# Optimization experiments

Hardware: AMD Instinct MI355X
Metric: run time of the kernel (lower is better)

The kernel has to match this reference:

```python
import jax, jax.numpy as jnp
import numpy as np

N_NODES = 100000
N_EDGES = 1600000
NODE_F = 8   # augmented node features
EDGE_F = 2   # augmented edge features
GLOB_F = 1
HID = 16
L = 3        # message passing steps

EDGE_IN = GLOB_F + EDGE_F + 2 * NODE_F   # 19
NODE_IN = GLOB_F + EDGE_F + NODE_F       # 11
GLOB_IN = EDGE_F + NODE_F + GLOB_F       # 11


def setup_inputs() -> dict:
    key = jax.random.key(0)
    ks = jax.random.split(key, 20)
    inp = {
        "x": jax.random.normal(ks[0], (N_NODES, NODE_F), dtype=jnp.float32),
        "edge_index": jax.random.randint(ks[1], (2, N_EDGES), 0, N_NODES, dtype=jnp.int32),
        "edge_attr": jax.random.normal(ks[2], (N_EDGES, EDGE_F), dtype=jnp.float32),
        "g": jax.random.normal(ks[3], (1, GLOB_F), dtype=jnp.float32),
    }
    s = 0.1
    inp["edge_W1"] = jax.random.normal(ks[4], (L, EDGE_IN, HID), dtype=jnp.float32) * s
    inp["edge_b1"] = jnp.zeros((L, HID), dtype=jnp.float32)
    inp["edge_W2"] = jax.random.normal(ks[5], (L, HID, EDGE_F), dtype=jnp.float32) * s
    inp["edge_b2"] = jnp.zeros((L, EDGE_F), dtype=jnp.float32)
    inp["node_W1"] = jax.random.normal(ks[6], (L, NODE_IN, HID), dtype=jnp.float32) * s
    inp["node_b1"] = jnp.zeros((L, HID), dtype=jnp.float32)
    inp["node_W2"] = jax.random.normal(ks[7], (L, HID, NODE_F), dtype=jnp.float32) * s
    inp["node_b2"] = jnp.zeros((L, NODE_F), dtype=jnp.float32)
    inp["glob_W1"] = jax.random.normal(ks[8], (L, GLOB_IN, HID), dtype=jnp.float32) * s
    inp["glob_b1"] = jnp.zeros((L, HID), dtype=jnp.float32)
    inp["glob_W2"] = jax.random.normal(ks[9], (L, HID, GLOB_F), dtype=jnp.float32) * s
    inp["glob_b2"] = jnp.zeros((L, GLOB_F), dtype=jnp.float32)
    return inp


def _mlp(h, W1, b1, W2, b2):
    # two-layer MLP with ReLU after first layer only (activate_final=False, no layer_norm)
    return jnp.maximum(h @ W1 + b1, 0.0) @ W2 + b2


def reference(x, edge_index, edge_attr, g,
              edge_W1, edge_b1, edge_W2, edge_b2,
              node_W1, node_b1, node_W2, node_b2,
              glob_W1, glob_b1, glob_W2, glob_b2):
    row, col = edge_index[0], edge_index[1]
    n = x.shape[0]
    for l in range(L):
        g_e = jnp.broadcast_to(g, (row.shape[0], GLOB_F))
        # edge block: gather node features along edges, concat, MLP -> [E, EDGE_F]
        e_in = jnp.concatenate([g_e, x[row], x[col], edge_attr], axis=1)
        edge_emb = _mlp(e_in, edge_W1[l], edge_b1[l], edge_W2[l], edge_b2[l])
        # sum-aggregate edge embeddings to source nodes
        agg = jax.ops.segment_sum(edge_emb, row, num_segments=n)
        g_n = jnp.broadcast_to(g, (n, GLOB_F))
        node_emb = _mlp(jnp.concatenate([g_n, x, agg], axis=1),
                        node_W1[l], node_b1[l], node_W2[l], node_b2[l])
        # global block on mean-aggregated edge/node embeddings
        edge_gl = jnp.mean(edge_emb, axis=0, keepdims=True)
        node_gl = jnp.mean(node_emb, axis=0, keepdims=True)
        g = _mlp(jnp.concatenate([node_gl, edge_gl, g], axis=1),
                 glob_W1[l], glob_b1[l], glob_W2[l], glob_b2[l])
        x, edge_attr = node_emb, edge_emb
    return x  # final node embeddings [N, NODE_F]
```

## Files before the change

### kernel.cpp

```cpp
#include <hip/hip_runtime.h>

#define NN 100000
#define NE 1600000
#define CH 4096
#define NCHUNK ((NE + CH - 1) / CH)
#define NBUCK ((NN + 255) / 256)

__device__ __forceinline__ float wave_red(float v) {
#pragma unroll
    for (int off = 32; off > 0; off >>= 1) v += __shfl_down(v, off, 64);
    return v;
}

__global__ __launch_bounds__(256) void hist_kernel(
    const int* __restrict__ ei, int* __restrict__ hist)
{
    __shared__ int h[NBUCK];
    int t = threadIdx.x, c = blockIdx.x;
    for (int b = t; b < NBUCK; b += 256) h[b] = 0;
    __syncthreads();
    int base = c * CH;
    for (int i = t; i < CH; i += 256) {
        int e = base + i;
        if (e < NE) atomicAdd(&h[ei[e] >> 8], 1);
    }
    __syncthreads();
    for (int b = t; b < NBUCK; b += 256) hist[c * NBUCK + b] = h[b];
}

__global__ __launch_bounds__(512) void bscan_kernel(
    const int* __restrict__ hist, int* __restrict__ baseT, int* __restrict__ colTotal)
{
    __shared__ int buf[2][512];
    int b = blockIdx.x, t = threadIdx.x;
    int v = (t < NCHUNK) ? hist[t * NBUCK + b] : 0;
    buf[0][t] = v;
    __syncthreads();
    int src = 0;
    for (int d = 1; d < 512; d <<= 1) {
        int nv = buf[src][t] + ((t >= d) ? buf[src][t - d] : 0);
        buf[src ^ 1][t] = nv;
        src ^= 1;
        __syncthreads();
    }
    if (t < NCHUNK) baseT[b * NCHUNK + t] = buf[src][t] - v;
    if (t == NCHUNK - 1) colTotal[b] = buf[src][t];
}

__global__ __launch_bounds__(512) void boff_kernel(
    const int* __restrict__ colTotal, int* __restrict__ b_off)
{
    __shared__ int buf[2][512];
    int t = threadIdx.x;
    int v = (t < NBUCK) ? colTotal[t] : 0;
    buf[0][t] = v;
    __syncthreads();
    int src = 0;
    for (int d = 1; d < 512; d <<= 1) {
        int nv = buf[src][t] + ((t >= d) ? buf[src][t - d] : 0);
        buf[src ^ 1][t] = nv;
        src ^= 1;
        __syncthreads();
    }
    if (t < NBUCK) b_off[t] = buf[src][t] - v;
    if (t == NBUCK - 1) b_off[NBUCK] = buf[src][t];
}

__global__ __launch_bounds__(256) void fillb_kernel(
    const int* __restrict__ ei, const float* __restrict__ eattr,
    const int* __restrict__ baseT, const int* __restrict__ b_off,
    float4* __restrict__ rec)
{
    __shared__ int sslot[NBUCK];
    int t = threadIdx.x, c = blockIdx.x;
    for (int b = t; b < NBUCK; b += 256)
        sslot[b] = b_off[b] + baseT[b * NCHUNK + c];
    __syncthreads();
    int base = c * CH;
    for (int i = t; i < CH; i += 256) {
        int e = base + i;
        if (e < NE) {
            int row = ei[e];
            int slot = atomicAdd(&sslot[row >> 8], 1);
            float2 ea = reinterpret_cast<const float2*>(eattr)[e];
            float4 v;
            v.x = __int_as_float(row);
            v.y = __int_as_float(ei[NE + e]);
            v.z = ea.x; v.w = ea.y;
            rec[slot] = v;
        }
    }
}

template <bool WRITE_REC, bool NEED_SUM>
__global__ __launch_bounds__(256, 4) void fused_kernel(
    float4* __restrict__ rec, const int* __restrict__ b_off,
    const float* __restrict__ gptr,
    const float* __restrict__ eW1, const float* __restrict__ eB1,
    const float* __restrict__ eW2, const float* __restrict__ eB2,
    const float* __restrict__ xin,
    const float* __restrict__ nW1, const float* __restrict__ nB1,
    const float* __restrict__ nW2, const float* __restrict__ nB2,
    float* __restrict__ xout, float* __restrict__ sums)
{
    __shared__ float sPrT[16 * 256];
    __shared__ float sagg[256][2];
    __shared__ float redE[4][2];
    __shared__ float redN[4][8];
    int tid = threadIdx.x;
    sagg[tid][0] = 0.f; sagg[tid][1] = 0.f;

    int n0 = blockIdx.x * 256;
    int nrow = n0 + tid;
    if (nrow < NN) {
        const float4* xi = reinterpret_cast<const float4*>(xin + (size_t)nrow * 8);
        float4 a0 = xi[0], a1 = xi[1];
        float xv[8] = {a0.x, a0.y, a0.z, a0.w, a1.x, a1.y, a1.z, a1.w};
        float pr[16];
#pragma unroll
        for (int q = 0; q < 16; q++) pr[q] = 0.f;
#pragma unroll
        for (int k = 0; k < 8; k++) {
            float v = xv[k];
#pragma unroll
            for (int q = 0; q < 16; q++) pr[q] += v * eW1[(1 + k) * 16 + q];
        }
#pragma unroll
        for (int q = 0; q < 16; q++) sPrT[q * 256 + tid] = pr[q];
    }
    __syncthreads();

    int e0 = b_off[blockIdx.x], e1 = b_off[blockIdx.x + 1];

    float gval = gptr[0];
    float gterm[16];
#pragma unroll
    for (int q = 0; q < 16; q++) gterm[q] = eB1[q] + gval * eW1[q];

    float t0 = 0.f, t1 = 0.f;
    for (int e = e0 + tid; e < e1; e += 256) {
        float4 r = rec[e];
        int row = __float_as_int(r.x);
        int col = __float_as_int(r.y);
        float ea0 = r.z, ea1 = r.w;
        int li = row - n0;
        const float4* xc4 = reinterpret_cast<const float4*>(xin + (size_t)col * 8);
        float4 c0 = xc4[0], c1 = xc4[1];
        float xc[8] = {c0.x, c0.y, c0.z, c0.w, c1.x, c1.y, c1.z, c1.w};
        float h[16];
#pragma unroll
        for (int q = 0; q < 16; q++) h[q] = gterm[q] + sPrT[q * 256 + li];
#pragma unroll
        for (int k = 0; k < 8; k++) {
            float v = xc[k];
#pragma unroll
            for (int q = 0; q < 16; q++) h[q] += v * eW1[(9 + k) * 16 + q];
        }
#pragma unroll
        for (int q = 0; q < 16; q++) {
            h[q] += ea0 * eW1[17 * 16 + q];
            h[q] += ea1 * eW1[18 * 16 + q];
        }
        float s0 = eB2[0], s1 = eB2[1];
#pragma unroll
        for (int q = 0; q < 16; q++) {
            float rr = fmaxf(h[q], 0.f);
            s0 += rr * eW2[2 * q];
            s1 += rr * eW2[2 * q + 1];
        }
        if (WRITE_REC) {
            float4 w;
            w.x = r.x; w.y = r.y; w.z = s0; w.w = s1;
            rec[e] = w;
        }
        atomicAdd(&sagg[li][0], s0);
        atomicAdd(&sagg[li][1], s1);
        t0 += s0; t1 += s1;
    }

    if (NEED_SUM) {
        float r0 = wave_red(t0);
        float r1 = wave_red(t1);
        int wave = tid >> 6, lane = tid & 63;
        if (lane == 0) { redE[wave][0] = r0; redE[wave][1] = r1; }
    }
    __syncthreads();
    if (NEED_SUM && tid == 0) {
        atomicAdd(&sums[0], redE[0][0] + redE[1][0] + redE[2][0] + redE[3][0]);
        atomicAdd(&sums[1], redE[0][1] + redE[1][1] + redE[2][1] + redE[3][1]);
    }

    int n = n0 + tid;
    float out[8];
#pragma unroll
    for (int m = 0; m < 8; m++) out[m] = 0.f;

    if (n < NN) {
        float in[11];
        in[0] = gval;
        const float4* xi = reinterpret_cast<const float4*>(xin + (size_t)n * 8);
        float4 a0 = xi[0], a1 = xi[1];
        in[1] = a0.x; in[2] = a0.y; in[3] = a0.z; in[4] = a0.w;
        in[5] = a1.x; in[6] = a1.y; in[7] = a1.z; in[8] = a1.w;
        in[9] = sagg[tid][0]; in[10] = sagg[tid][1];

        float h[16];
#pragma unroll
        for (int q = 0; q < 16; q++) h[q] = nB1[q];
#pragma unroll
        for (int k = 0; k < 11; k++) {
            float v = in[k];
#pragma unroll
            for (int q = 0; q < 16; q++) h[q] += v * nW1[k * 16 + q];
        }
#pragma unroll
        for (int m = 0; m < 8; m++) out[m] = nB2[m];
#pragma unroll
        for (int q = 0; q < 16; q++) {
            float hq = fmaxf(h[q], 0.f);
#pragma unroll
            for (int m = 0; m < 8; m++) out[m] += hq * nW2[q * 8 + m];
        }
        float4* xo = reinterpret_cast<float4*>(xout + (size_t)n * 8);
        xo[0] = make_float4(out[0], out[1], out[2], out[3]);
        xo[1] = make_float4(out[4], out[5], out[6], out[7]);
    }
    if (NEED_SUM) {
        float r[8];
#pragma unroll
        for (int m = 0; m < 8; m++) r[m] = wave_red(out[m]);
        int wave = tid >> 6, lane = tid & 63;
        if (lane == 0) {
#pragma unroll
            for (int m = 0; m < 8; m++) redN[wave][m] = r[m];
        }
        __syncthreads();
        if (tid == 0) {
#pragma unroll
            for (int m = 0; m < 8; m++) {
                float s = redN[0][m] + redN[1][m] + redN[2][m] + redN[3][m];
                atomicAdd(&sums[2 + m], s);
            }
        }
    }
}

__global__ void glob_kernel(const float* __restrict__ sums,
                            const float* __restrict__ gold,
                            const float* __restrict__ W1, const float* __restrict__ B1,
                            const float* __restrict__ W2, const float* __restrict__ B2,
                            float* __restrict__ gnew)
{
    if (threadIdx.x == 0 && blockIdx.x == 0) {
        float in[11];
#pragma unroll
        for (int j = 0; j < 8; j++) in[j] = sums[2 + j] * (1.0f / NN);
        in[8] = sums[0] * (1.0f / NE);
        in[9] = sums[1] * (1.0f / NE);
        in[10] = gold[0];
        float acc = B2[0];
#pragma unroll
        for (int j = 0; j < 16; j++) {
            float h = B1[j];
#pragma unroll
            for (int k = 0; k < 11; k++) h += in[k] * W1[k * 16 + j];
            acc += fmaxf(h, 0.f) * W2[j];
        }
        gnew[0] = acc;
    }
}

extern "C" void kernel_launch(void* const* d_in, const int* in_sizes, int n_in,
                              void* d_out, int out_size, void* d_ws, size_t ws_size,
                              hipStream_t stream) {
    const float* x     = (const float*)d_in[0];
    const int*   ei    = (const int*)d_in[1];
    const float* eattr = (const float*)d_in[2];
    const float* g     = (const float*)d_in[3];
    const float* eW1 = (const float*)d_in[4];
    const float* eB1 = (const float*)d_in[5];
    const float* eW2 = (const float*)d_in[6];
    const float* eB2 = (const float*)d_in[7];
    const float* nW1 = (const float*)d_in[8];
    const float* nB1 = (const float*)d_in[9];
    const float* nW2 = (const float*)d_in[10];
    const float* nB2 = (const float*)d_in[11];
    const float* gW1 = (const float*)d_in[12];
    const float* gB1 = (const float*)d_in[13];
    const float* gW2 = (const float*)d_in[14];
    const float* gB2 = (const float*)d_in[15];
    float* out = (float*)d_out;

    char* ws = (char*)d_ws;
    float*  xb0   = (float*)(ws);
    float*  xb1   = (float*)(ws + 3200000);
    int*    b_off = (int*)  (ws + 6400000);
    float*  sums  = (float*)(ws + 6401600);
    float*  g1    = (float*)(ws + 6401728);
    float*  g2    = g1 + 1;
    float4* rec   = (float4*)(ws + 6401792);
    int*    hist     = (int*)xb1;
    int*    baseT    = (int*)((char*)xb1 + 611584);
    int*    colTotal = (int*)((char*)xb1 + 1223168);

    dim3 blk(256);
    dim3 cgrid(NCHUNK);
    dim3 bgrid(NBUCK);
    dim3 ngrid((NN + 255) / 256);

    hipMemsetAsync(sums, 0, 128, stream);
    hist_kernel<<<cgrid, blk, 0, stream>>>(ei, hist);
    bscan_kernel<<<bgrid, 512, 0, stream>>>(hist, baseT, colTotal);
    boff_kernel<<<1, 512, 0, stream>>>(colTotal, b_off);
    fillb_kernel<<<cgrid, blk, 0, stream>>>(ei, eattr, baseT, b_off, rec);

    fused_kernel<true, true><<<bgrid, blk, 0, stream>>>(
        rec, b_off, g,
        eW1, eB1, eW2, eB2,
        x, nW1, nB1, nW2, nB2,
        xb0, sums);
    glob_kernel<<<1, 64, 0, stream>>>(sums, g, gW1, gB1, gW2, gB2, g1);

    fused_kernel<true, true><<<bgrid, blk, 0, stream>>>(
        rec, b_off, g1,
        eW1 + 304, eB1 + 16, eW2 + 32, eB2 + 2,
        xb0, nW1 + 176, nB1 + 16, nW2 + 128, nB2 + 8,
        xb1, sums + 16);
    glob_kernel<<<1, 64, 0, stream>>>(sums + 16, g1, gW1 + 176, gB1 + 16, gW2 + 16, gB2 + 1, g2);

    fused_kernel<false, false><<<bgrid, blk, 0, stream>>>(
        rec, b_off, g2,
        eW1 + 608, eB1 + 32, eW2 + 64, eB2 + 4,
        xb1, nW1 + 352, nB1 + 32, nW2 + 256, nB2 + 16,
        out, sums);
}
```

Measured before the change: 354.9 us.

## Replace bucket-sorted fused edge/node kernel with unsorted edge kernel plus global atomics

Drops the histogram, scan and fill passes that bucketed edges by source node. Edges are now processed in their original order by a grid-stride edge kernel that gathers both endpoint features and scatters into global agg buffers with global float atomics. A separate node kernel then reads those buffers. This removes the sort preprocessing and the per-bucket load imbalance, but adds an extra row gather per edge, global atomics, a memset of the agg buffers, and an extra launch per layer.

```diff
diff --git a/kernel.cpp b/kernel.cpp
--- a/kernel.cpp
+++ b/kernel.cpp
@@ -2,9 +2,8 @@
 
 #define NN 100000
 #define NE 1600000
-#define CH 4096
-#define NCHUNK ((NE + CH - 1) / CH)
-#define NBUCK ((NN + 255) / 256)
+#define EGRID 2048
+#define NGRID ((NN + 255) / 256)
 
 __device__ __forceinline__ float wave_red(float v) {
 #pragma unroll
@@ -12,197 +11,102 @@
     return v;
 }
 
-__global__ __launch_bounds__(256) void hist_kernel(
-    const int* __restrict__ ei, int* __restrict__ hist)
-{
-    __shared__ int h[NBUCK];
-    int t = threadIdx.x, c = blockIdx.x;
-    for (int b = t; b < NBUCK; b += 256) h[b] = 0;
-    __syncthreads();
-    int base = c * CH;
-    for (int i = t; i < CH; i += 256) {
-        int e = base + i;
-        if (e < NE) atomicAdd(&h[ei[e] >> 8], 1);
-    }
-    __syncthreads();
-    for (int b = t; b < NBUCK; b += 256) hist[c * NBUCK + b] = h[b];
-}
-
-__global__ __launch_bounds__(512) void bscan_kernel(
-    const int* __restrict__ hist, int* __restrict__ baseT, int* __restrict__ colTotal)
-{
-    __shared__ int buf[2][512];
-    int b = blockIdx.x, t = threadIdx.x;
-    int v = (t < NCHUNK) ? hist[t * NBUCK + b] : 0;
-    buf[0][t] = v;
-    __syncthreads();
-    int src = 0;
-    for (int d = 1; d < 512; d <<= 1) {
-        int nv = buf[src][t] + ((t >= d) ? buf[src][t - d] : 0);
-        buf[src ^ 1][t] = nv;
-        src ^= 1;
-        __syncthreads();
-    }
-    if (t < NCHUNK) baseT[b * NCHUNK + t] = buf[src][t] - v;
-    if (t == NCHUNK - 1) colTotal[b] = buf[src][t];
-}
-
-__global__ __launch_bounds__(512) void boff_kernel(
-    const int* __restrict__ colTotal, int* __restrict__ b_off)
-{
-    __shared__ int buf[2][512];
-    int t = threadIdx.x;
-    int v = (t < NBUCK) ? colTotal[t] : 0;
-    buf[0][t] = v;
-    __syncthreads();
-    int src = 0;
-    for (int d = 1; d < 512; d <<= 1) {
-        int nv = buf[src][t] + ((t >= d) ? buf[src][t - d] : 0);
-        buf[src ^ 1][t] = nv;
-        src ^= 1;
-        __syncthreads();
-    }
-    if (t < NBUCK) b_off[t] = buf[src][t] - v;
-    if (t == NBUCK - 1) b_off[NBUCK] = buf[src][t];
-}
-
-__global__ __launch_bounds__(256) void fillb_kernel(
-    const int* __restrict__ ei, const float* __restrict__ eattr,
-    const int* __restrict__ baseT, const int* __restrict__ b_off,
-    float4* __restrict__ rec)
-{
-    __shared__ int sslot[NBUCK];
-    int t = threadIdx.x, c = blockIdx.x;
-    for (int b = t; b < NBUCK; b += 256)
-        sslot[b] = b_off[b] + baseT[b * NCHUNK + c];
-    __syncthreads();
-    int base = c * CH;
-    for (int i = t; i < CH; i += 256) {
-        int e = base + i;
-        if (e < NE) {
-            int row = ei[e];
-            int slot = atomicAdd(&sslot[row >> 8], 1);
-            float2 ea = reinterpret_cast<const float2*>(eattr)[e];
-            float4 v;
-            v.x = __int_as_float(row);
-            v.y = __int_as_float(ei[NE + e]);
-            v.z = ea.x; v.w = ea.y;
-            rec[slot] = v;
-        }
-    }
-}
-
-template <bool WRITE_REC, bool NEED_SUM>
-__global__ __launch_bounds__(256, 4) void fused_kernel(
-    float4* __restrict__ rec, const int* __restrict__ b_off,
+template <bool WRITE_EMB, bool NEED_SUM>
+__global__ __launch_bounds__(256) void edge_kernel(
+    const int* __restrict__ ei,
+    const float2* __restrict__ eain,
+    float2* __restrict__ eout,
+    const float* __restrict__ xin,
     const float* __restrict__ gptr,
     const float* __restrict__ eW1, const float* __restrict__ eB1,
     const float* __restrict__ eW2, const float* __restrict__ eB2,
-    const float* __restrict__ xin,
+    float* __restrict__ agg, float* __restrict__ sums)
+{
+    __shared__ float redE[4][2];
+    int tid = threadIdx.x;
+    float gval = gptr[0];
+    float gterm[16];
+#pragma unroll
+    for (int q = 0; q < 16; q++) gterm[q] = eB1[q] + gval * eW1[q];
+
+    float t0 = 0.f, t1 = 0.f;
+    for (int e = blockIdx.x * 256 + tid; e < NE; e += EGRID * 256) {
+        int row = ei[e];
+        int col = ei[NE + e];
+        float2 ea = eain[e];
+        const float4* xr4 = reinterpret_cast<const float4*>(xin + (size_t)row * 8);
+        float4 r0 = xr4[0], r1 = xr4[1];
+        const float4* xc4 = reinterpret_cast<const float4*>(xin + (size_t)col * 8);
+        float4 c0 = xc4[0], c1 = xc4[1];
+        float xr[8] = {r0.x, r0.y, r0.z, r0.w, r1.x, r1.y, r1.z, r1.w};
+        float xc[8] = {c0.x, c0.y, c0.z, c0.w, c1.x, c1.y, c1.z, c1.w};
+        float h[16];
+#pragma unroll
+        for (int q = 0; q < 16; q++) h[q] = gterm[q];
+#pragma unroll
+        for (int k = 0; k < 8; k++) {
+            float vr = xr[k], vc = xc[k];
+#pragma unroll
+            for (int q = 0; q < 16; q++) {
+                h[q] += vr * eW1[(1 + k) * 16 + q];
+                h[q] += vc * eW1[(9 + k) * 16 + q];
+            }
+        }
+#pragma unroll
+        for (int q = 0; q < 16; q++) {
+            h[q] += ea.x * eW1[17 * 16 + q];
+            h[q] += ea.y * eW1[18 * 16 + q];
+        }
+        float s0 = eB2[0], s1 = eB2[1];
+#pragma unroll
+        for (int q = 0; q < 16; q++) {
+            float rr = fmaxf(h[q], 0.f);
+            s0 += rr * eW2[2 * q];
+            s1 += rr * eW2[2 * q + 1];
+        }
+        if (WRITE_EMB) eout[e] = make_float2(s0, s1);
+        atomicAdd(&agg[(size_t)row * 2],     s0);
+        atomicAdd(&agg[(size_t)row * 2 + 1], s1);
+        t0 += s0; t1 += s1;
+    }
+
+    if (NEED_SUM) {
+        float r0 = wave_red(t0), r1 = wave_red(t1);
+        int wave = tid >> 6, lane = tid & 63;
+        if (lane == 0) { redE[wave][0] = r0; redE[wave][1] = r1; }
+        __syncthreads();
+        if (tid == 0) {
+            atomicAdd(&sums[0], redE[0][0] + redE[1][0] + redE[2][0] + redE[3][0]);
+            atomicAdd(&sums[1], redE[0][1] + redE[1][1] + redE[2][1] + redE[3][1]);
+        }
+    }
+}
+
+template <bool NEED_SUM>
+__global__ __launch_bounds__(256) void node_kernel(
+    const float* __restrict__ xin, const float* __restrict__ agg,
+    const float* __restrict__ gptr,
     const float* __restrict__ nW1, const float* __restrict__ nB1,
     const float* __restrict__ nW2, const float* __restrict__ nB2,
     float* __restrict__ xout, float* __restrict__ sums)
 {
-    __shared__ float sPrT[16 * 256];
-    __shared__ float sagg[256][2];
-    __shared__ float redE[4][2];
     __shared__ float redN[4][8];
     int tid = threadIdx.x;
-    sagg[tid][0] = 0.f; sagg[tid][1] = 0.f;
-
-    int n0 = blockIdx.x * 256;
-    int nrow = n0 + tid;
-    if (nrow < NN) {
-        const float4* xi = reinterpret_cast<const float4*>(xin + (size_t)nrow * 8);
-        float4 a0 = xi[0], a1 = xi[1];
-        float xv[8] = {a0.x, a0.y, a0.z, a0.w, a1.x, a1.y, a1.z, a1.w};
-        float pr[16];
-#pragma unroll
-        for (int q = 0; q < 16; q++) pr[q] = 0.f;
-#pragma unroll
-        for (int k = 0; k < 8; k++) {
-            float v = xv[k];
-#pragma unroll
-            for (int q = 0; q < 16; q++) pr[q] += v * eW1[(1 + k) * 16 + q];
-        }
-#pragma unroll
-        for (int q = 0; q < 16; q++) sPrT[q * 256 + tid] = pr[q];
-    }
-    __syncthreads();
-
-    int e0 = b_off[blockIdx.x], e1 = b_off[blockIdx.x + 1];
-
-    float gval = gptr[0];
-    float gterm[16];
-#pragma unroll
-    for (int q = 0; q < 16; q++) gterm[q] = eB1[q] + gval * eW1[q];
-
-    float t0 = 0.f, t1 = 0.f;
-    for (int e = e0 + tid; e < e1; e += 256) {
-        float4 r = rec[e];
-        int row = __float_as_int(r.x);
-        int col = __float_as_int(r.y);
-        float ea0 = r.z, ea1 = r.w;
-        int li = row - n0;
-        const float4* xc4 = reinterpret_cast<const float4*>(xin + (size_t)col * 8);
-        float4 c0 = xc4[0], c1 = xc4[1];
-        float xc[8] = {c0.x, c0.y, c0.z, c0.w, c1.x, c1.y, c1.z, c1.w};
-        float h[16];
-#pragma unroll
-        for (int q = 0; q < 16; q++) h[q] = gterm[q] + sPrT[q * 256 + li];
-#pragma unroll
-        for (int k = 0; k < 8; k++) {
-            float v = xc[k];
-#pragma unroll
-            for (int q = 0; q < 16; q++) h[q] += v * eW1[(9 + k) * 16 + q];
-        }
-#pragma unroll
-        for (int q = 0; q < 16; q++) {
-            h[q] += ea0 * eW1[17 * 16 + q];
-            h[q] += ea1 * eW1[18 * 16 + q];
-        }
-        float s0 = eB2[0], s1 = eB2[1];
-#pragma unroll
-        for (int q = 0; q < 16; q++) {
-            float rr = fmaxf(h[q], 0.f);
-            s0 += rr * eW2[2 * q];
-            s1 += rr * eW2[2 * q + 1];
-        }
-        if (WRITE_REC) {
-            float4 w;
-            w.x = r.x; w.y = r.y; w.z = s0; w.w = s1;
-            rec[e] = w;
-        }
-        atomicAdd(&sagg[li][0], s0);
-        atomicAdd(&sagg[li][1], s1);
-        t0 += s0; t1 += s1;
-    }
-
-    if (NEED_SUM) {
-        float r0 = wave_red(t0);
-        float r1 = wave_red(t1);
-        int wave = tid >> 6, lane = tid & 63;
-        if (lane == 0) { redE[wave][0] = r0; redE[wave][1] = r1; }
-    }
-    __syncthreads();
-    if (NEED_SUM && tid == 0) {
-        atomicAdd(&sums[0], redE[0][0] + redE[1][0] + redE[2][0] + redE[3][0]);
-        atomicAdd(&sums[1], redE[0][1] + redE[1][1] + redE[2][1] + redE[3][1]);
-    }
-
-    int n = n0 + tid;
+    int n = blockIdx.x * 256 + tid;
     float out[8];
 #pragma unroll
     for (int m = 0; m < 8; m++) out[m] = 0.f;
 
     if (n < NN) {
+        float gval = gptr[0];
         float in[11];
         in[0] = gval;
         const float4* xi = reinterpret_cast<const float4*>(xin + (size_t)n * 8);
         float4 a0 = xi[0], a1 = xi[1];
         in[1] = a0.x; in[2] = a0.y; in[3] = a0.z; in[4] = a0.w;
         in[5] = a1.x; in[6] = a1.y; in[7] = a1.z; in[8] = a1.w;
-        in[9] = sagg[tid][0]; in[10] = sagg[tid][1];
+        float2 ag = reinterpret_cast<const float2*>(agg)[n];
+        in[9] = ag.x; in[10] = ag.y;
 
         float h[16];
 #pragma unroll
@@ -292,45 +196,38 @@
     float* out = (float*)d_out;
 
     char* ws = (char*)d_ws;
-    float*  xb0   = (float*)(ws);
-    float*  xb1   = (float*)(ws + 3200000);
-    int*    b_off = (int*)  (ws + 6400000);
-    float*  sums  = (float*)(ws + 6401600);
-    float*  g1    = (float*)(ws + 6401728);
-    float*  g2    = g1 + 1;
-    float4* rec   = (float4*)(ws + 6401792);
-    int*    hist     = (int*)xb1;
-    int*    baseT    = (int*)((char*)xb1 + 611584);
-    int*    colTotal = (int*)((char*)xb1 + 1223168);
+    float*  xb0  = (float*)(ws);
+    float*  xb1  = (float*)(ws + 3200000);
+    float*  sums = (float*)(ws + 6400000);
+    float*  g1   = (float*)(ws + 6400128);
+    float*  g2   = g1 + 1;
+    float*  agg0 = (float*)(ws + 6400256);
+    float*  agg1 = (float*)(ws + 7200256);
+    float*  agg2 = (float*)(ws + 8000256);
+    float2* eemb = (float2*)(ws + 8800256);
 
     dim3 blk(256);
-    dim3 cgrid(NCHUNK);
-    dim3 bgrid(NBUCK);
-    dim3 ngrid((NN + 255) / 256);
 
     hipMemsetAsync(sums, 0, 128, stream);
-    hist_kernel<<<cgrid, blk, 0, stream>>>(ei, hist);
-    bscan_kernel<<<bgrid, 512, 0, stream>>>(hist, baseT, colTotal);
-    boff_kernel<<<1, 512, 0, stream>>>(colTotal, b_off);
-    fillb_kernel<<<cgrid, blk, 0, stream>>>(ei, eattr, baseT, b_off, rec);
-
-    fused_kernel<true, true><<<bgrid, blk, 0, stream>>>(
-        rec, b_off, g,
-        eW1, eB1, eW2, eB2,
-        x, nW1, nB1, nW2, nB2,
-        xb0, sums);
+    hipMemsetAsync(agg0, 0, 3 * 800000, stream);
+
+    edge_kernel<true, true><<<EGRID, blk, 0, stream>>>(
+        ei, (const float2*)eattr, eemb, x, g,
+        eW1, eB1, eW2, eB2, agg0, sums);
+    node_kernel<true><<<NGRID, blk, 0, stream>>>(
+        x, agg0, g, nW1, nB1, nW2, nB2, xb0, sums);
     glob_kernel<<<1, 64, 0, stream>>>(sums, g, gW1, gB1, gW2, gB2, g1);
 
-    fused_kernel<true, true><<<bgrid, blk, 0, stream>>>(
-        rec, b_off, g1,
-        eW1 + 304, eB1 + 16, eW2 + 32, eB2 + 2,
-        xb0, nW1 + 176, nB1 + 16, nW2 + 128, nB2 + 8,
-        xb1, sums + 16);
+    edge_kernel<true, true><<<EGRID, blk, 0, stream>>>(
+        ei, eemb, eemb, xb0, g1,
+        eW1 + 304, eB1 + 16, eW2 + 32, eB2 + 2, agg1, sums + 16);
+    node_kernel<true><<<NGRID, blk, 0, stream>>>(
+        xb0, agg1, g1, nW1 + 176, nB1 + 16, nW2 + 128, nB2 + 8, xb1, sums + 16);
     glob_kernel<<<1, 64, 0, stream>>>(sums + 16, g1, gW1 + 176, gB1 + 16, gW2 + 16, gB2 + 1, g2);
 
-    fused_kernel<false, false><<<bgrid, blk, 0, stream>>>(
-        rec, b_off, g2,
-        eW1 + 608, eB1 + 32, eW2 + 64, eB2 + 4,
-        xb1, nW1 + 352, nB1 + 32, nW2 + 256, nB2 + 16,
-        out, sums);
-}
+    edge_kernel<false, false><<<EGRID, blk, 0, stream>>>(
+        ei, eemb, nullptr, xb1, g2,
+        eW1 + 608, eB1 + 32, eW2 + 64, eB2 + 4, agg2, sums);
+    node_kernel<false><<<NGRID, blk, 0, stream>>>(
+        xb1, agg2, g2, nW1 + 352, nB1 + 32, nW2 + 256, nB2 + 16, out, sums);
+}
```

After: 745.4 us. +110.0%, slower.

## Shrink node buckets to 64 and split edge records into packed key plus attrs

Applied to the files above, without the earlier changes.

Node buckets shrink from 256 to 64 nodes, so the fused edge/node kernel launches about four times as many blocks. The per-bucket offset scan is widened to 1024 threads to cover the larger bucket count. Each 16-byte edge record becomes a 4-byte key (local row packed with the column index) plus a separate float2 of attributes, which cuts streamed and rewritten edge traffic per layer. The node pass reuses the x values already loaded at the start, the occupancy hint is dropped, and the shared-memory cross-wave node reduction is removed. In exchange, only 64 of 256 threads do node work per block, and the preprocessing scans handle larger histograms.

```diff
diff --git a/kernel.cpp b/kernel.cpp
--- a/kernel.cpp
+++ b/kernel.cpp
@@ -4,7 +4,8 @@
 #define NE 1600000
 #define CH 4096
 #define NCHUNK ((NE + CH - 1) / CH)
-#define NBUCK ((NN + 255) / 256)
+#define BUCK 64
+#define NBUCK ((NN + BUCK - 1) / BUCK)
 
 __device__ __forceinline__ float wave_red(float v) {
 #pragma unroll
@@ -22,7 +23,7 @@
     int base = c * CH;
     for (int i = t; i < CH; i += 256) {
         int e = base + i;
-        if (e < NE) atomicAdd(&h[ei[e] >> 8], 1);
+        if (e < NE) atomicAdd(&h[ei[e] >> 6], 1);
     }
     __syncthreads();
     for (int b = t; b < NBUCK; b += 256) hist[c * NBUCK + b] = h[b];
@@ -47,29 +48,33 @@
     if (t == NCHUNK - 1) colTotal[b] = buf[src][t];
 }
 
-__global__ __launch_bounds__(512) void boff_kernel(
+__global__ __launch_bounds__(1024) void boff_kernel(
     const int* __restrict__ colTotal, int* __restrict__ b_off)
 {
-    __shared__ int buf[2][512];
+    __shared__ int buf[2][2048];
     int t = threadIdx.x;
-    int v = (t < NBUCK) ? colTotal[t] : 0;
-    buf[0][t] = v;
+    for (int i = t; i < 2048; i += 1024)
+        buf[0][i] = (i < NBUCK) ? colTotal[i] : 0;
     __syncthreads();
     int src = 0;
-    for (int d = 1; d < 512; d <<= 1) {
-        int nv = buf[src][t] + ((t >= d) ? buf[src][t - d] : 0);
-        buf[src ^ 1][t] = nv;
+    for (int d = 1; d < 2048; d <<= 1) {
+        for (int i = t; i < 2048; i += 1024) {
+            int v = buf[src][i];
+            if (i >= d) v += buf[src][i - d];
+            buf[src ^ 1][i] = v;
+        }
         src ^= 1;
         __syncthreads();
     }
-    if (t < NBUCK) b_off[t] = buf[src][t] - v;
-    if (t == NBUCK - 1) b_off[NBUCK] = buf[src][t];
+    for (int i = t; i < 2048; i += 1024)
+        if (i < NBUCK) b_off[i] = buf[src][i] - colTotal[i];
+    if (t == 0) b_off[NBUCK] = buf[src][NBUCK - 1];
 }
 
 __global__ __launch_bounds__(256) void fillb_kernel(
     const int* __restrict__ ei, const float* __restrict__ eattr,
     const int* __restrict__ baseT, const int* __restrict__ b_off,
-    float4* __restrict__ rec)
+    int* __restrict__ key, float2* __restrict__ recEA)
 {
     __shared__ int sslot[NBUCK];
     int t = threadIdx.x, c = blockIdx.x;
@@ -81,20 +86,18 @@
         int e = base + i;
         if (e < NE) {
             int row = ei[e];
-            int slot = atomicAdd(&sslot[row >> 8], 1);
+            int slot = atomicAdd(&sslot[row >> 6], 1);
             float2 ea = reinterpret_cast<const float2*>(eattr)[e];
-            float4 v;
-            v.x = __int_as_float(row);
-            v.y = __int_as_float(ei[NE + e]);
-            v.z = ea.x; v.w = ea.y;
-            rec[slot] = v;
+            key[slot] = ((row & (BUCK - 1)) << 17) | ei[NE + e];
+            recEA[slot] = ea;
         }
     }
 }
 
 template <bool WRITE_REC, bool NEED_SUM>
-__global__ __launch_bounds__(256, 4) void fused_kernel(
-    float4* __restrict__ rec, const int* __restrict__ b_off,
+__global__ __launch_bounds__(256) void fused_kernel(
+    const int* __restrict__ key, float2* __restrict__ recEA,
+    const int* __restrict__ b_off,
     const float* __restrict__ gptr,
     const float* __restrict__ eW1, const float* __restrict__ eB1,
     const float* __restrict__ eW2, const float* __restrict__ eB2,
@@ -103,19 +106,21 @@
     const float* __restrict__ nW2, const float* __restrict__ nB2,
     float* __restrict__ xout, float* __restrict__ sums)
 {
-    __shared__ float sPrT[16 * 256];
-    __shared__ float sagg[256][2];
+    __shared__ float sPrT[16 * BUCK];
+    __shared__ float sagg[BUCK][2];
     __shared__ float redE[4][2];
-    __shared__ float redN[4][8];
     int tid = threadIdx.x;
-    sagg[tid][0] = 0.f; sagg[tid][1] = 0.f;
-
-    int n0 = blockIdx.x * 256;
-    int nrow = n0 + tid;
-    if (nrow < NN) {
-        const float4* xi = reinterpret_cast<const float4*>(xin + (size_t)nrow * 8);
+    if (tid < 2 * BUCK) ((float*)sagg)[tid] = 0.f;
+
+    int n0 = blockIdx.x * BUCK;
+    float gval = gptr[0];
+    float xv[8];
+    bool own = (tid < BUCK) && (n0 + tid < NN);
+    if (own) {
+        const float4* xi = reinterpret_cast<const float4*>(xin + (size_t)(n0 + tid) * 8);
         float4 a0 = xi[0], a1 = xi[1];
-        float xv[8] = {a0.x, a0.y, a0.z, a0.w, a1.x, a1.y, a1.z, a1.w};
+        xv[0] = a0.x; xv[1] = a0.y; xv[2] = a0.z; xv[3] = a0.w;
+        xv[4] = a1.x; xv[5] = a1.y; xv[6] = a1.z; xv[7] = a1.w;
         float pr[16];
 #pragma unroll
         for (int q = 0; q < 16; q++) pr[q] = 0.f;
@@ -126,40 +131,38 @@
             for (int q = 0; q < 16; q++) pr[q] += v * eW1[(1 + k) * 16 + q];
         }
 #pragma unroll
-        for (int q = 0; q < 16; q++) sPrT[q * 256 + tid] = pr[q];
+        for (int q = 0; q < 16; q++) sPrT[q * BUCK + tid] = pr[q];
     }
     __syncthreads();
 
     int e0 = b_off[blockIdx.x], e1 = b_off[blockIdx.x + 1];
 
-    float gval = gptr[0];
     float gterm[16];
 #pragma unroll
     for (int q = 0; q < 16; q++) gterm[q] = eB1[q] + gval * eW1[q];
 
     float t0 = 0.f, t1 = 0.f;
     for (int e = e0 + tid; e < e1; e += 256) {
-        float4 r = rec[e];
-        int row = __float_as_int(r.x);
-        int col = __float_as_int(r.y);
-        float ea0 = r.z, ea1 = r.w;
-        int li = row - n0;
+        int k = key[e];
+        int col = k & 0x1FFFF;
+        int li = k >> 17;
+        float2 ea = recEA[e];
         const float4* xc4 = reinterpret_cast<const float4*>(xin + (size_t)col * 8);
         float4 c0 = xc4[0], c1 = xc4[1];
         float xc[8] = {c0.x, c0.y, c0.z, c0.w, c1.x, c1.y, c1.z, c1.w};
         float h[16];
 #pragma unroll
-        for (int q = 0; q < 16; q++) h[q] = gterm[q] + sPrT[q * 256 + li];
-#pragma unroll
-        for (int k = 0; k < 8; k++) {
-            float v = xc[k];
-#pragma unroll
-            for (int q = 0; q < 16; q++) h[q] += v * eW1[(9 + k) * 16 + q];
+        for (int q = 0; q < 16; q++) h[q] = gterm[q] + sPrT[q * BUCK + li];
+#pragma unroll
+        for (int kk = 0; kk < 8; kk++) {
+            float v = xc[kk];
+#pragma unroll
+            for (int q = 0; q < 16; q++) h[q] += v * eW1[(9 + kk) * 16 + q];
         }
 #pragma unroll
         for (int q = 0; q < 16; q++) {
-            h[q] += ea0 * eW1[17 * 16 + q];
-            h[q] += ea1 * eW1[18 * 16 + q];
+            h[q] += ea.x * eW1[17 * 16 + q];
+            h[q] += ea.y * eW1[18 * 16 + q];
         }
         float s0 = eB2[0], s1 = eB2[1];
 #pragma unroll
@@ -168,19 +171,14 @@
             s0 += rr * eW2[2 * q];
             s1 += rr * eW2[2 * q + 1];
         }
-        if (WRITE_REC) {
-            float4 w;
-            w.x = r.x; w.y = r.y; w.z = s0; w.w = s1;
-            rec[e] = w;
-        }
+        if (WRITE_REC) recEA[e] = make_float2(s0, s1);
         atomicAdd(&sagg[li][0], s0);
         atomicAdd(&sagg[li][1], s1);
         t0 += s0; t1 += s1;
     }
 
     if (NEED_SUM) {
-        float r0 = wave_red(t0);
-        float r1 = wave_red(t1);
+        float r0 = wave_red(t0), r1 = wave_red(t1);
         int wave = tid >> 6, lane = tid & 63;
         if (lane == 0) { redE[wave][0] = r0; redE[wave][1] = r1; }
     }
@@ -190,18 +188,16 @@
         atomicAdd(&sums[1], redE[0][1] + redE[1][1] + redE[2][1] + redE[3][1]);
     }
 
-    int n = n0 + tid;
     float out[8];
 #pragma unroll
     for (int m = 0; m < 8; m++) out[m] = 0.f;
 
-    if (n < NN) {
+    if (own) {
+        int n = n0 + tid;
         float in[11];
         in[0] = gval;
-        const float4* xi = reinterpret_cast<const float4*>(xin + (size_t)n * 8);
-        float4 a0 = xi[0], a1 = xi[1];
-        in[1] = a0.x; in[2] = a0.y; in[3] = a0.z; in[4] = a0.w;
-        in[5] = a1.x; in[6] = a1.y; in[7] = a1.z; in[8] = a1.w;
+#pragma unroll
+        for (int k = 0; k < 8; k++) in[1 + k] = xv[k];
         in[9] = sagg[tid][0]; in[10] = sagg[tid][1];
 
         float h[16];
@@ -229,18 +225,9 @@
         float r[8];
 #pragma unroll
         for (int m = 0; m < 8; m++) r[m] = wave_red(out[m]);
-        int wave = tid >> 6, lane = tid & 63;
-        if (lane == 0) {
-#pragma unroll
-            for (int m = 0; m < 8; m++) redN[wave][m] = r[m];
-        }
-        __syncthreads();
         if (tid == 0) {
 #pragma unroll
-            for (int m = 0; m < 8; m++) {
-                float s = redN[0][m] + redN[1][m] + redN[2][m] + redN[3][m];
-                atomicAdd(&sums[2 + m], s);
-            }
+            for (int m = 0; m < 8; m++) atomicAdd(&sums[2 + m], r[m]);
         }
     }
 }
@@ -295,41 +282,41 @@
     float*  xb0   = (float*)(ws);
     float*  xb1   = (float*)(ws + 3200000);
     int*    b_off = (int*)  (ws + 6400000);
-    float*  sums  = (float*)(ws + 6401600);
-    float*  g1    = (float*)(ws + 6401728);
+    float*  sums  = (float*)(ws + 6406400);
+    float*  g1    = (float*)(ws + 6406528);
     float*  g2    = g1 + 1;
-    float4* rec   = (float4*)(ws + 6401792);
-    int*    hist     = (int*)xb1;
-    int*    baseT    = (int*)((char*)xb1 + 611584);
-    int*    colTotal = (int*)((char*)xb1 + 1223168);
+    int*    key   = (int*)  (ws + 6406656);
+    float2* recEA = (float2*)(ws + 12806656);
+    int*    hist     = (int*)ws;
+    int*    baseT    = (int*)(ws + 2444800);
+    int*    colTotal = (int*)(ws + 4889600);
 
     dim3 blk(256);
     dim3 cgrid(NCHUNK);
     dim3 bgrid(NBUCK);
-    dim3 ngrid((NN + 255) / 256);
 
     hipMemsetAsync(sums, 0, 128, stream);
     hist_kernel<<<cgrid, blk, 0, stream>>>(ei, hist);
     bscan_kernel<<<bgrid, 512, 0, stream>>>(hist, baseT, colTotal);
-    boff_kernel<<<1, 512, 0, stream>>>(colTotal, b_off);
-    fillb_kernel<<<cgrid, blk, 0, stream>>>(ei, eattr, baseT, b_off, rec);
+    boff_kernel<<<1, 1024, 0, stream>>>(colTotal, b_off);
+    fillb_kernel<<<cgrid, blk, 0, stream>>>(ei, eattr, baseT, b_off, key, recEA);
 
     fused_kernel<true, true><<<bgrid, blk, 0, stream>>>(
-        rec, b_off, g,
+        key, recEA, b_off, g,
         eW1, eB1, eW2, eB2,
         x, nW1, nB1, nW2, nB2,
         xb0, sums);
     glob_kernel<<<1, 64, 0, stream>>>(sums, g, gW1, gB1, gW2, gB2, g1);
 
     fused_kernel<true, true><<<bgrid, blk, 0, stream>>>(
-        rec, b_off, g1,
+        key, recEA, b_off, g1,
         eW1 + 304, eB1 + 16, eW2 + 32, eB2 + 2,
         xb0, nW1 + 176, nB1 + 16, nW2 + 128, nB2 + 8,
         xb1, sums + 16);
     glob_kernel<<<1, 64, 0, stream>>>(sums + 16, g1, gW1 + 176, gB1 + 16, gW2 + 16, gB2 + 1, g2);
 
     fused_kernel<false, false><<<bgrid, blk, 0, stream>>>(
-        rec, b_off, g2,
+        key, recEA, b_off, g2,
         eW1 + 608, eB1 + 32, eW2 + 64, eB2 + 4,
         xb1, nW1 + 352, nB1 + 32, nW2 + 256, nB2 + 16,
         out, sums);
```

Result: slower. 680.5 us (+91.7%).

## Split fused edge/node kernel and subdivide each bucket's edges across four blocks

Applied to the files above, without the earlier changes.

The fused per-bucket kernel is split into an edge kernel launched with four blocks per 256-node bucket, each handling a quarter of that bucket's edges and writing partial aggregates to a global buffer. A separate node kernel sums the four partials and runs the node MLP. Edge weights are also preloaded into registers, and the per-node precomputed features move to a row-major, float4-readable shared layout. The goal is more parallelism for the edge phase, which had only about 391 blocks. The cost is extra launches, a global round-trip for partial aggregates, redundant per-block node precompute, and high register pressure under launch_bounds(256,1).

```diff
diff --git a/kernel.cpp b/kernel.cpp
--- a/kernel.cpp
+++ b/kernel.cpp
@@ -5,6 +5,7 @@
 #define CH 4096
 #define NCHUNK ((NE + CH - 1) / CH)
 #define NBUCK ((NN + 255) / 256)
+#define SUB 4
 
 __device__ __forceinline__ float wave_red(float v) {
 #pragma unroll
@@ -92,25 +93,24 @@
     }
 }
 
-template <bool WRITE_REC, bool NEED_SUM>
-__global__ __launch_bounds__(256, 4) void fused_kernel(
+template <bool WRITE_EMB, bool NEED_SUM>
+__global__ __launch_bounds__(256, 1) void edge_kernel(
     float4* __restrict__ rec, const int* __restrict__ b_off,
     const float* __restrict__ gptr,
     const float* __restrict__ eW1, const float* __restrict__ eB1,
     const float* __restrict__ eW2, const float* __restrict__ eB2,
     const float* __restrict__ xin,
-    const float* __restrict__ nW1, const float* __restrict__ nB1,
-    const float* __restrict__ nW2, const float* __restrict__ nB2,
-    float* __restrict__ xout, float* __restrict__ sums)
-{
-    __shared__ float sPrT[16 * 256];
+    float2* __restrict__ pagg, float* __restrict__ sums)
+{
+    __shared__ float sPr[256][20];
     __shared__ float sagg[256][2];
     __shared__ float redE[4][2];
-    __shared__ float redN[4][8];
     int tid = threadIdx.x;
+    int b = blockIdx.x >> 2, s = blockIdx.x & 3;
+    int n0 = b << 8;
     sagg[tid][0] = 0.f; sagg[tid][1] = 0.f;
 
-    int n0 = blockIdx.x * 256;
+    float gval = gptr[0];
     int nrow = n0 + tid;
     if (nrow < NN) {
         const float4* xi = reinterpret_cast<const float4*>(xin + (size_t)nrow * 8);
@@ -125,84 +125,127 @@
 #pragma unroll
             for (int q = 0; q < 16; q++) pr[q] += v * eW1[(1 + k) * 16 + q];
         }
-#pragma unroll
-        for (int q = 0; q < 16; q++) sPrT[q * 256 + tid] = pr[q];
-    }
-    __syncthreads();
-
-    int e0 = b_off[blockIdx.x], e1 = b_off[blockIdx.x + 1];
-
-    float gval = gptr[0];
-    float gterm[16];
-#pragma unroll
-    for (int q = 0; q < 16; q++) gterm[q] = eB1[q] + gval * eW1[q];
+        float4* pw = reinterpret_cast<float4*>(&sPr[tid][0]);
+#pragma unroll
+        for (int t4 = 0; t4 < 4; t4++)
+            pw[t4] = make_float4(pr[4*t4], pr[4*t4+1], pr[4*t4+2], pr[4*t4+3]);
+    }
+    __syncthreads();
+
+    float cw[128], aw[32], ow[32], gterm[16];
+    {
+        const float4* W4 = reinterpret_cast<const float4*>(eW1 + 9 * 16);
+#pragma unroll
+        for (int i = 0; i < 32; i++) {
+            float4 w = W4[i];
+            cw[4*i] = w.x; cw[4*i+1] = w.y; cw[4*i+2] = w.z; cw[4*i+3] = w.w;
+        }
+        const float4* A4 = reinterpret_cast<const float4*>(eW1 + 17 * 16);
+#pragma unroll
+        for (int i = 0; i < 8; i++) {
+            float4 w = A4[i];
+            aw[4*i] = w.x; aw[4*i+1] = w.y; aw[4*i+2] = w.z; aw[4*i+3] = w.w;
+        }
+        const float4* O4 = reinterpret_cast<const float4*>(eW2);
+#pragma unroll
+        for (int i = 0; i < 8; i++) {
+            float4 w = O4[i];
+            ow[4*i] = w.x; ow[4*i+1] = w.y; ow[4*i+2] = w.z; ow[4*i+3] = w.w;
+        }
+#pragma unroll
+        for (int q = 0; q < 16; q++) gterm[q] = eB1[q] + gval * eW1[q];
+    }
+    float b20 = eB2[0], b21 = eB2[1];
+
+    int e0b = b_off[b], e1b = b_off[b + 1];
+    int qlen = (e1b - e0b + SUB - 1) / SUB;
+    int es = e0b + s * qlen;
+    int ee = min(e1b, es + qlen);
 
     float t0 = 0.f, t1 = 0.f;
-    for (int e = e0 + tid; e < e1; e += 256) {
+    for (int e = es + tid; e < ee; e += 256) {
         float4 r = rec[e];
-        int row = __float_as_int(r.x);
+        int li  = __float_as_int(r.x) - n0;
         int col = __float_as_int(r.y);
-        float ea0 = r.z, ea1 = r.w;
-        int li = row - n0;
         const float4* xc4 = reinterpret_cast<const float4*>(xin + (size_t)col * 8);
         float4 c0 = xc4[0], c1 = xc4[1];
+        const float4* pr4 = reinterpret_cast<const float4*>(&sPr[li][0]);
+        float4 p0 = pr4[0], p1 = pr4[1], p2 = pr4[2], p3 = pr4[3];
+        float h[16];
+        h[0]  = gterm[0]  + p0.x; h[1]  = gterm[1]  + p0.y;
+        h[2]  = gterm[2]  + p0.z; h[3]  = gterm[3]  + p0.w;
+        h[4]  = gterm[4]  + p1.x; h[5]  = gterm[5]  + p1.y;
+        h[6]  = gterm[6]  + p1.z; h[7]  = gterm[7]  + p1.w;
+        h[8]  = gterm[8]  + p2.x; h[9]  = gterm[9]  + p2.y;
+        h[10] = gterm[10] + p2.z; h[11] = gterm[11] + p2.w;
+        h[12] = gterm[12] + p3.x; h[13] = gterm[13] + p3.y;
+        h[14] = gterm[14] + p3.z; h[15] = gterm[15] + p3.w;
         float xc[8] = {c0.x, c0.y, c0.z, c0.w, c1.x, c1.y, c1.z, c1.w};
-        float h[16];
-#pragma unroll
-        for (int q = 0; q < 16; q++) h[q] = gterm[q] + sPrT[q * 256 + li];
 #pragma unroll
         for (int k = 0; k < 8; k++) {
             float v = xc[k];
 #pragma unroll
-            for (int q = 0; q < 16; q++) h[q] += v * eW1[(9 + k) * 16 + q];
-        }
-#pragma unroll
-        for (int q = 0; q < 16; q++) {
-            h[q] += ea0 * eW1[17 * 16 + q];
-            h[q] += ea1 * eW1[18 * 16 + q];
-        }
-        float s0 = eB2[0], s1 = eB2[1];
+            for (int q = 0; q < 16; q++) h[q] += v * cw[k * 16 + q];
+        }
+#pragma unroll
+        for (int q = 0; q < 16; q++) h[q] += r.z * aw[q] + r.w * aw[16 + q];
+        float s0 = b20, s1 = b21;
 #pragma unroll
         for (int q = 0; q < 16; q++) {
             float rr = fmaxf(h[q], 0.f);
-            s0 += rr * eW2[2 * q];
-            s1 += rr * eW2[2 * q + 1];
-        }
-        if (WRITE_REC) {
-            float4 w;
-            w.x = r.x; w.y = r.y; w.z = s0; w.w = s1;
-            rec[e] = w;
-        }
+            s0 += rr * ow[2 * q];
+            s1 += rr * ow[2 * q + 1];
+        }
+        if (WRITE_EMB) rec[e] = make_float4(r.x, r.y, s0, s1);
         atomicAdd(&sagg[li][0], s0);
         atomicAdd(&sagg[li][1], s1);
         t0 += s0; t1 += s1;
     }
 
     if (NEED_SUM) {
-        float r0 = wave_red(t0);
-        float r1 = wave_red(t1);
+        float r0 = wave_red(t0), r1 = wave_red(t1);
         int wave = tid >> 6, lane = tid & 63;
         if (lane == 0) { redE[wave][0] = r0; redE[wave][1] = r1; }
     }
     __syncthreads();
+    pagg[((size_t)s * NBUCK + b) * 256 + tid] =
+        make_float2(sagg[tid][0], sagg[tid][1]);
     if (NEED_SUM && tid == 0) {
         atomicAdd(&sums[0], redE[0][0] + redE[1][0] + redE[2][0] + redE[3][0]);
         atomicAdd(&sums[1], redE[0][1] + redE[1][1] + redE[2][1] + redE[3][1]);
     }
-
-    int n = n0 + tid;
+}
+
+template <bool NEED_SUM>
+__global__ __launch_bounds__(256) void node_kernel(
+    const float* __restrict__ xin, const float2* __restrict__ pagg,
+    const float* __restrict__ gptr,
+    const float* __restrict__ nW1, const float* __restrict__ nB1,
+    const float* __restrict__ nW2, const float* __restrict__ nB2,
+    float* __restrict__ xout, float* __restrict__ sums)
+{
+    __shared__ float redN[4][8];
+    int tid = threadIdx.x, b = blockIdx.x;
+    int n = b * 256 + tid;
     float out[8];
 #pragma unroll
     for (int m = 0; m < 8; m++) out[m] = 0.f;
 
     if (n < NN) {
+        float ag0 = 0.f, ag1 = 0.f;
+#pragma unroll
+        for (int s = 0; s < SUB; s++) {
+            float2 p = pagg[((size_t)s * NBUCK + b) * 256 + tid];
+            ag0 += p.x; ag1 += p.y;
+        }
+        float gval = gptr[0];
         float in[11];
         in[0] = gval;
         const float4* xi = reinterpret_cast<const float4*>(xin + (size_t)n * 8);
         float4 a0 = xi[0], a1 = xi[1];
         in[1] = a0.x; in[2] = a0.y; in[3] = a0.z; in[4] = a0.w;
         in[5] = a1.x; in[6] = a1.y; in[7] = a1.z; in[8] = a1.w;
-        in[9] = sagg[tid][0]; in[10] = sagg[tid][1];
+        in[9] = ag0; in[10] = ag1;
 
         float h[16];
 #pragma unroll
@@ -299,6 +342,7 @@
     float*  g1    = (float*)(ws + 6401728);
     float*  g2    = g1 + 1;
     float4* rec   = (float4*)(ws + 6401792);
+    float2* pagg  = (float2*)(ws + 32001792);
     int*    hist     = (int*)xb1;
     int*    baseT    = (int*)((char*)xb1 + 611584);
     int*    colTotal = (int*)((char*)xb1 + 1223168);
@@ -306,7 +350,7 @@
     dim3 blk(256);
     dim3 cgrid(NCHUNK);
     dim3 bgrid(NBUCK);
-    dim3 ngrid((NN + 255) / 256);
+    dim3 egrid(NBUCK * SUB);
 
     hipMemsetAsync(sums, 0, 128, stream);
     hist_kernel<<<cgrid, blk, 0, stream>>>(ei, hist);
@@ -314,23 +358,20 @@
     boff_kernel<<<1, 512, 0, stream>>>(colTotal, b_off);
     fillb_kernel<<<cgrid, blk, 0, stream>>>(ei, eattr, baseT, b_off, rec);
 
-    fused_kernel<true, true><<<bgrid, blk, 0, stream>>>(
-        rec, b_off, g,
-        eW1, eB1, eW2, eB2,
-        x, nW1, nB1, nW2, nB2,
-        xb0, sums);
+    edge_kernel<true, true><<<egrid, blk, 0, stream>>>(
+        rec, b_off, g, eW1, eB1, eW2, eB2, x, pagg, sums);
+    node_kernel<true><<<bgrid, blk, 0, stream>>>(
+        x, pagg, g, nW1, nB1, nW2, nB2, xb0, sums);
     glob_kernel<<<1, 64, 0, stream>>>(sums, g, gW1, gB1, gW2, gB2, g1);
 
-    fused_kernel<true, true><<<bgrid, blk, 0, stream>>>(
-        rec, b_off, g1,
-        eW1 + 304, eB1 + 16, eW2 + 32, eB2 + 2,
-        xb0, nW1 + 176, nB1 + 16, nW2 + 128, nB2 + 8,
-        xb1, sums + 16);
+    edge_kernel<true, true><<<egrid, blk, 0, stream>>>(
+        rec, b_off, g1, eW1 + 304, eB1 + 16, eW2 + 32, eB2 + 2, xb0, pagg, sums + 16);
+    node_kernel<true><<<bgrid, blk, 0, stream>>>(
+        xb0, pagg, g1, nW1 + 176, nB1 + 16, nW2 + 128, nB2 + 8, xb1, sums + 16);
     glob_kernel<<<1, 64, 0, stream>>>(sums + 16, g1, gW1 + 176, gB1 + 16, gW2 + 16, gB2 + 1, g2);
 
-    fused_kernel<false, false><<<bgrid, blk, 0, stream>>>(
-        rec, b_off, g2,
-        eW1 + 608, eB1 + 32, eW2 + 64, eB2 + 4,
-        xb1, nW1 + 352, nB1 + 32, nW2 + 256, nB2 + 16,
-        out, sums);
-}
+    edge_kernel<false, false><<<egrid, blk, 0, stream>>>(
+        rec, b_off, g2, eW1 + 608, eB1 + 32, eW2 + 64, eB2 + 4, xb1, pagg, sums);
+    node_kernel<false><<<bgrid, blk, 0, stream>>>(
+        xb1, pagg, g2, nW1 + 352, nB1 + 32, nW2 + 256, nB2 + 16, out, sums);
+}
```

Measured after the change: 388.0 us. 9.3% more time.
